# Kernel optimization log

Measured on AMD Instinct MI355X. Metric: run time of the kernel, lower is better.

## Reference

```python
import jax, jax.numpy as jnp
import numpy as np

B, INPUT_LEN, F_IN = 32, 4096, 256
N = B * INPUT_LEN          # 131072 total nodes in the flattened batch
E = 4_194_304              # ~avg degree 32
HID, OUT = 3, 1            # GCNConv(256->3) then GCNConv(3->1), per source code
PRED_LEN = 1024


def setup_inputs() -> dict:
    key = jax.random.key(0)
    k = jax.random.split(key, 5)
    node_features = jax.random.normal(k[0], (B, INPUT_LEN, F_IN), dtype=jnp.float32)
    # flattened, already-offset edge index (Batch.from_data_list result)
    edge_index = jax.random.randint(k[1], (2, E), 0, N, dtype=jnp.int32)
    W1 = jax.random.normal(k[2], (F_IN, HID), dtype=jnp.float32) / np.float32(np.sqrt(F_IN))
    b1 = jnp.zeros((HID,), dtype=jnp.float32)
    W2 = jax.random.normal(k[3], (HID, OUT), dtype=jnp.float32) / np.float32(np.sqrt(HID))
    b2 = jnp.zeros((OUT,), dtype=jnp.float32)
    return {"node_features": node_features, "W1": W1, "b1": b1, "W2": W2, "b2": b2,
            "edge_index": edge_index, "pred_len": PRED_LEN, "input_len": INPUT_LEN}


def _gcn_norm(edge_index, num_nodes, dtype):
    # PyG gcn_norm: add self-loops, deg over destination, symmetric deg^-1/2 norm
    loop = jnp.arange(num_nodes, dtype=edge_index.dtype)
    src = jnp.concatenate([edge_index[0], loop])
    dst = jnp.concatenate([edge_index[1], loop])
    deg = jax.ops.segment_sum(jnp.ones_like(src, dtype=dtype), dst, num_segments=num_nodes)
    dinv = jnp.where(deg > 0, jax.lax.rsqrt(deg), 0.0).astype(dtype)
    norm = dinv[src] * dinv[dst]  # [E+N]
    return src, dst, norm


def _gcn_conv(x, src, dst, norm, W, b, num_nodes):
    h = x @ W                              # [N, out] linear first (small out dim)
    msg = h[src] * norm[:, None]           # gather + scale per edge
    out = jax.ops.segment_sum(msg, dst, num_segments=num_nodes)  # scatter-add
    return out + b


def reference(node_features, W1, b1, W2, b2, edge_index, pred_len, input_len):
    n_nodes = node_features.shape[0] * node_features.shape[1]
    x = node_features.reshape(n_nodes, node_features.shape[2])
    src, dst, norm = _gcn_norm(edge_index, n_nodes, x.dtype)
    h = jax.nn.relu(_gcn_conv(x, src, dst, norm, W1, b1, n_nodes))
    h = _gcn_conv(h, src, dst, norm, W2, b2, n_nodes)
    h = h.reshape(-1, input_len, h.shape[1])   # [B, input_len, num_target]
    return h[:, :pred_len, :]
```

## Files before the change

### kernel.cpp

```cpp
#include <hip/hip_runtime.h>
#include <stdint.h>

#define F_IN 256
#define QSCALE 512.0f
#define QBIAS  8192
#define FMASK  0x1FFFFFull
#define H2Q    16384.0f
#define NBUK   256
#define BSH    9
#define BMASK  511u
#define LCAP   48
#define NCHUNK 512
#define EPB    8192
#define BSLOTS (NCHUNK * LCAP)
#define OVF_CAP 256
#define SENT   0xFFFFFFFFu
#define XBUF_SZ ((size_t)NBUK * BSLOTS * 4)
#define OVF_SZ  ((size_t)NBUK * OVF_CAP * 4)

__device__ __forceinline__ float bf2f(unsigned short u) {
    union { unsigned int i; float f; } v; v.i = ((unsigned int)u) << 16; return v.f;
}
__device__ __forceinline__ unsigned short f2bf(float f) {
    union { unsigned int i; float f; } v; v.f = f;
    unsigned int r = v.i + 0x7FFF + ((v.i >> 16) & 1);
    return (unsigned short)(r >> 16);
}
__device__ __forceinline__ unsigned long long packq(float v0, float v1, float v2) {
    int m0 = __float2int_rn(v0 * QSCALE);
    int m1 = __float2int_rn(v1 * QSCALE);
    int m2 = __float2int_rn(v2 * QSCALE);
    m0 = max(-4095, min(4095, m0));
    m1 = max(-4095, min(4095, m1));
    m2 = max(-4095, min(4095, m2));
    return (unsigned long long)(unsigned)(m0 + QBIAS)
         | ((unsigned long long)(unsigned)(m1 + QBIAS) << 21)
         | ((unsigned long long)(unsigned)(m2 + QBIAS) << 42);
}

__global__ void k_init(unsigned int* __restrict__ gcur,
                       const unsigned int* __restrict__ w1w, int* __restrict__ flag) {
    __shared__ int cnt;
    if (threadIdx.x == 0) cnt = 0;
    for (int i = threadIdx.x; i < NBUK * 16; i += blockDim.x) gcur[i] = 0u;
    __syncthreads();
    int local = 0;
    for (int i = threadIdx.x; i < 384; i += blockDim.x) {
        unsigned e = (w1w[i] >> 7) & 0xFF;
        if (e >= 100 && e <= 135) local++;
    }
    atomicAdd(&cnt, local);
    __syncthreads();
    if (threadIdx.x == 0) *flag = (2 * cnt < 384) ? 1 : 0;
}

__global__ void __launch_bounds__(256, 8)
k_gemv(const void* __restrict__ xv_, const void* __restrict__ w1_,
       unsigned short* __restrict__ h1out, const int* __restrict__ flag, int N) {
    __shared__ float wlds[F_IN * 3];
    int f32mode = *flag;
    if (f32mode) {
        const float* w = (const float*)w1_;
        for (int i = threadIdx.x; i < F_IN * 3; i += 256) wlds[i] = w[i];
    } else {
        const unsigned short* w = (const unsigned short*)w1_;
        for (int i = threadIdx.x; i < F_IN * 3; i += 256) wlds[i] = bf2f(w[i]);
    }
    __syncthreads();
    int wave = threadIdx.x >> 6, lane = threadIdx.x & 63;
    int g = lane >> 3, e = lane & 7;
    int row = blockIdx.x * 32 + wave * 8 + g;
    if (row >= N) return;
    float p0 = 0.f, p1 = 0.f, p2 = 0.f;
    if (f32mode) {
        const float4* xr = (const float4*)((const float*)xv_ + (size_t)row * F_IN);
        float4 xv[8];
        #pragma unroll
        for (int j = 0; j < 8; j++) xv[j] = xr[e + 8 * j];
        #pragma unroll
        for (int j = 0; j < 8; j++) {
            int f = 4 * e + 32 * j;
            const float4* wp = (const float4*)&wlds[f * 3];
            float4 wa = wp[0], wb = wp[1], wc = wp[2];
            p0 += xv[j].x*wa.x + xv[j].y*wa.w + xv[j].z*wb.z + xv[j].w*wc.y;
            p1 += xv[j].x*wa.y + xv[j].y*wb.x + xv[j].z*wb.w + xv[j].w*wc.z;
            p2 += xv[j].x*wa.z + xv[j].y*wb.y + xv[j].z*wc.x + xv[j].w*wc.w;
        }
    } else {
        const ushort4* xr = (const ushort4*)((const unsigned short*)xv_ + (size_t)row * F_IN);
        ushort4 xv[8];
        #pragma unroll
        for (int j = 0; j < 8; j++) xv[j] = xr[e + 8 * j];
        #pragma unroll
        for (int j = 0; j < 8; j++) {
            int f = 4 * e + 32 * j;
            const float4* wp = (const float4*)&wlds[f * 3];
            float4 wa = wp[0], wb = wp[1], wc = wp[2];
            float x0 = bf2f(xv[j].x), x1 = bf2f(xv[j].y),
                  x2 = bf2f(xv[j].z), x3 = bf2f(xv[j].w);
            p0 += x0*wa.x + x1*wa.w + x2*wb.z + x3*wc.y;
            p1 += x0*wa.y + x1*wb.x + x2*wb.w + x3*wc.z;
            p2 += x0*wa.z + x1*wb.y + x2*wc.x + x3*wc.w;
        }
    }
    #pragma unroll
    for (int m = 1; m < 8; m <<= 1) {
        p0 += __shfl_xor(p0, m, 64);
        p1 += __shfl_xor(p1, m, 64);
        p2 += __shfl_xor(p2, m, 64);
    }
    if (e == 0) {
        ushort4 o;
        o.x = f2bf(p0); o.y = f2bf(p1); o.z = f2bf(p2); o.w = 0;
        ((ushort4*)h1out)[row] = o;
    }
}

__global__ void __launch_bounds__(1024, 8)
k_bucket(const int* __restrict__ src, const int* __restrict__ dst,
         unsigned int* __restrict__ xbuf, unsigned int* __restrict__ ovf,
         unsigned int* __restrict__ gcur) {
    __shared__ unsigned int lbuf[NBUK][LCAP];
    __shared__ unsigned int lcnt[NBUK];
    int b = blockIdx.x;
    for (int i = threadIdx.x; i < NBUK; i += 1024) lcnt[i] = 0u;
    __syncthreads();
    int g4 = b * 2048 + threadIdx.x;
    int4 sa = ((const int4*)src)[g4];
    int4 da = ((const int4*)dst)[g4];
    int4 sb = ((const int4*)src)[g4 + 1024];
    int4 db = ((const int4*)dst)[g4 + 1024];
    int ss[8] = {sa.x, sa.y, sa.z, sa.w, sb.x, sb.y, sb.z, sb.w};
    int dd[8] = {da.x, da.y, da.z, da.w, db.x, db.y, db.z, db.w};
    #pragma unroll
    for (int u = 0; u < 8; u++) {
        unsigned p = ((unsigned)ss[u] << BSH) | ((unsigned)dd[u] & BMASK);
        int bk = ((unsigned)dd[u]) >> BSH;
        unsigned lp = atomicAdd(&lcnt[bk], 1u);
        if (lp < LCAP) lbuf[bk][lp] = p;
        else {
            unsigned g = atomicAdd(&gcur[bk << 4], 1u);
            if (g < OVF_CAP) ovf[(size_t)bk * OVF_CAP + g] = p;
        }
    }
    __syncthreads();
    int wave = threadIdx.x >> 6, lane = threadIdx.x & 63;
    #pragma unroll
    for (int k = 0; k < 16; k++) {
        int bk = wave * 16 + k;
        unsigned c = min(lcnt[bk], (unsigned)LCAP);
        if (lane < 12) {
            uint4 v = *(const uint4*)&lbuf[bk][lane * 4];
            unsigned s0 = lane * 4;
            uint4 o;
            o.x = (s0 + 0 < c) ? v.x : SENT;
            o.y = (s0 + 1 < c) ? v.y : SENT;
            o.z = (s0 + 2 < c) ? v.z : SENT;
            o.w = (s0 + 3 < c) ? v.w : SENT;
            ((uint4*)(xbuf + ((size_t)bk * NCHUNK + b) * LCAP))[lane] = o;
        }
    }
}

__global__ void __launch_bounds__(1024, 8)
k_hist_pack(const unsigned int* __restrict__ xbuf, const unsigned int* __restrict__ ovf,
            const unsigned int* __restrict__ gcur,
            unsigned char* __restrict__ deg8, float* __restrict__ dinv,
            unsigned long long* __restrict__ h1con) {
    __shared__ unsigned int cnt[512];
    int B = blockIdx.x;
    for (int i = threadIdx.x; i < 512; i += 1024) cnt[i] = 0u;
    __syncthreads();
    const uint4* bp = (const uint4*)(xbuf + (size_t)B * BSLOTS);
    for (int i = threadIdx.x; i < BSLOTS / 4; i += 1024) {
        uint4 v = bp[i];
        if (v.x != SENT) atomicAdd(&cnt[v.x & BMASK], 1u);
        if (v.y != SENT) atomicAdd(&cnt[v.y & BMASK], 1u);
        if (v.z != SENT) atomicAdd(&cnt[v.z & BMASK], 1u);
        if (v.w != SENT) atomicAdd(&cnt[v.w & BMASK], 1u);
    }
    unsigned oc = min(gcur[B << 4], (unsigned)OVF_CAP);
    for (unsigned i = threadIdx.x; i < oc; i += 1024)
        atomicAdd(&cnt[ovf[(size_t)B * OVF_CAP + i] & BMASK], 1u);
    __syncthreads();
    if (threadIdx.x < 512) {
        int n = (B << BSH) | threadIdx.x;
        unsigned deg = 1u + cnt[threadIdx.x];
        deg8[n] = (unsigned char)min(deg, 255u);
        float dv = rsqrtf((float)deg);
        dinv[n] = dv;
        ushort4 h = ((const ushort4*)h1con)[n];
        h1con[n] = packq(bf2f(h.x) * dv, bf2f(h.y) * dv, bf2f(h.z) * dv);
    }
}

__global__ void __launch_bounds__(1024, 8)
k_scat1_lin2(const unsigned int* __restrict__ xbuf, const unsigned int* __restrict__ ovf,
             const unsigned int* __restrict__ gcur,
             const unsigned long long* __restrict__ con,
             const unsigned char* __restrict__ deg8, const float* __restrict__ dinv,
             const void* __restrict__ b1_, const void* __restrict__ w2_,
             int* __restrict__ h2q, const int* __restrict__ flag) {
    __shared__ unsigned long long acc[512];
    int B = blockIdx.x;
    for (int i = threadIdx.x; i < 512; i += 1024) acc[i] = 0ull;
    __syncthreads();
    const uint4* bp = (const uint4*)(xbuf + (size_t)B * BSLOTS);
    for (int i = threadIdx.x; i < BSLOTS / 4; i += 1024) {
        uint4 v = bp[i];
        unsigned i0 = (v.x == SENT) ? 0u : (v.x >> BSH);
        unsigned i1 = (v.y == SENT) ? 0u : (v.y >> BSH);
        unsigned i2 = (v.z == SENT) ? 0u : (v.z >> BSH);
        unsigned i3 = (v.w == SENT) ? 0u : (v.w >> BSH);
        unsigned long long c0 = con[i0], c1 = con[i1], c2 = con[i2], c3 = con[i3];
        if (v.x != SENT) atomicAdd(&acc[v.x & BMASK], c0);
        if (v.y != SENT) atomicAdd(&acc[v.y & BMASK], c1);
        if (v.z != SENT) atomicAdd(&acc[v.z & BMASK], c2);
        if (v.w != SENT) atomicAdd(&acc[v.w & BMASK], c3);
    }
    unsigned oc = min(gcur[B << 4], (unsigned)OVF_CAP);
    for (unsigned i = threadIdx.x; i < oc; i += 1024) {
        unsigned p = ovf[(size_t)B * OVF_CAP + i];
        atomicAdd(&acc[p & BMASK], con[p >> BSH]);
    }
    __syncthreads();
    if (threadIdx.x < 512) {
        int n = (B << BSH) | threadIdx.x;
        int f32mode = *flag;
        float b10, b11, b12, w20, w21, w22;
        if (f32mode) {
            const float* b1 = (const float*)b1_; const float* w2 = (const float*)w2_;
            b10 = b1[0]; b11 = b1[1]; b12 = b1[2];
            w20 = w2[0]; w21 = w2[1]; w22 = w2[2];
        } else {
            const unsigned short* b1 = (const unsigned short*)b1_;
            const unsigned short* w2 = (const unsigned short*)w2_;
            b10 = bf2f(b1[0]); b11 = bf2f(b1[1]); b12 = bf2f(b1[2]);
            w20 = bf2f(w2[0]); w21 = bf2f(w2[1]); w22 = bf2f(w2[2]);
        }
        unsigned long long T = acc[threadIdx.x] + con[n];
        long long dbias = (long long)deg8[n] * QBIAS;
        float q = 1.0f / QSCALE;
        float s0 = (float)((long long)( T        & FMASK) - dbias) * q;
        float s1 = (float)((long long)((T >> 21) & FMASK) - dbias) * q;
        float s2 = (float)((long long)((T >> 42) & FMASK) - dbias) * q;
        float dv = dinv[n];
        float a0 = fmaxf(s0 * dv + b10, 0.0f);
        float a1 = fmaxf(s1 * dv + b11, 0.0f);
        float a2 = fmaxf(s2 * dv + b12, 0.0f);
        float h2 = (a0 * w20 + a1 * w21 + a2 * w22) * dv;
        h2q[n] = __float2int_rn(h2 * H2Q);
    }
}

__global__ void __launch_bounds__(1024, 8)
k_scat2_out(const unsigned int* __restrict__ xbuf, const unsigned int* __restrict__ ovf,
            const unsigned int* __restrict__ gcur,
            const int* __restrict__ h2q, const float* __restrict__ dinv,
            const void* __restrict__ b2_, void* __restrict__ out_,
            const int* __restrict__ flag) {
    __shared__ int acc[512];
    int ob = blockIdx.x;
    int B = ((ob >> 1) << 3) | (ob & 1);
    for (int i = threadIdx.x; i < 512; i += 1024) acc[i] = 0;
    __syncthreads();
    const uint4* bp = (const uint4*)(xbuf + (size_t)B * BSLOTS);
    for (int i = threadIdx.x; i < BSLOTS / 4; i += 1024) {
        uint4 v = bp[i];
        unsigned i0 = (v.x == SENT) ? 0u : (v.x >> BSH);
        unsigned i1 = (v.y == SENT) ? 0u : (v.y >> BSH);
        unsigned i2 = (v.z == SENT) ? 0u : (v.z >> BSH);
        unsigned i3 = (v.w == SENT) ? 0u : (v.w >> BSH);
        int h0 = h2q[i0], h1 = h2q[i1], h2v = h2q[i2], h3 = h2q[i3];
        if (v.x != SENT) atomicAdd(&acc[v.x & BMASK], h0);
        if (v.y != SENT) atomicAdd(&acc[v.y & BMASK], h1);
        if (v.z != SENT) atomicAdd(&acc[v.z & BMASK], h2v);
        if (v.w != SENT) atomicAdd(&acc[v.w & BMASK], h3);
    }
    unsigned oc = min(gcur[B << 4], (unsigned)OVF_CAP);
    for (unsigned i = threadIdx.x; i < oc; i += 1024) {
        unsigned p = ovf[(size_t)B * OVF_CAP + i];
        atomicAdd(&acc[p & BMASK], h2q[p >> BSH]);
    }
    __syncthreads();
    if (threadIdx.x < 512) {
        int i = threadIdx.x;
        int n = (B << BSH) | i;
        int f32mode = *flag;
        float b2 = f32mode ? ((const float*)b2_)[0] : bf2f(((const unsigned short*)b2_)[0]);
        int S = h2q[n] + acc[i];
        float v = (float)S * (1.0f / H2Q) * dinv[n] + b2;
        int t = ((B >> 3) << 10) | ((B & 1) << 9) | i;
        if (f32mode) ((float*)out_)[t] = v;
        else         ((unsigned short*)out_)[t] = f2bf(v);
    }
}

extern "C" void kernel_launch(void* const* d_in, const int* in_sizes, int n_in,
                              void* d_out, int out_size, void* d_ws, size_t ws_size,
                              hipStream_t stream) {
    void*       x   = d_in[0];
    const void* w1  = d_in[1];
    const void* b1  = d_in[2];
    const void* w2  = d_in[3];
    const void* b2  = d_in[4];
    const int* eidx = (const int*)d_in[5];

    const int N = in_sizes[0] / F_IN;
    const int E = in_sizes[5] / 2;
    const int* src = eidx;
    const int* dst = eidx + E;

    char* ws = (char*)d_ws;
    unsigned char*      deg8  = (unsigned char*)(ws);
    float*              dinv  = (float*)(ws + (size_t)N);
    unsigned long long* h1con = (unsigned long long*)(ws + (size_t)5*N);
    int*                h2q   = (int*)(ws + (size_t)13*N);
    int*                flag  = (int*)(ws + (size_t)17*N);
    unsigned int*       gcur  = (unsigned int*)(ws + (size_t)17*N + 64);

    bool big_ws = ws_size >= ((size_t)(4u << 20) + XBUF_SZ + OVF_SZ);
    char* scratch = big_ws ? (ws + (4u << 20)) : (char*)x;
    unsigned int* xbuf = (unsigned int*)scratch;
    unsigned int* ovf  = (unsigned int*)(scratch + XBUF_SZ);

    int gemvB = N / 32;
    k_init<<<1, 256, 0, stream>>>(gcur, (const unsigned int*)w1, flag);
    if (big_ws) {
        k_bucket<<<NCHUNK, 1024, 0, stream>>>(src, dst, xbuf, ovf, gcur);
        k_gemv<<<gemvB, 256, 0, stream>>>(x, w1, (unsigned short*)h1con, flag, N);
    } else {
        k_gemv<<<gemvB, 256, 0, stream>>>(x, w1, (unsigned short*)h1con, flag, N);
        k_bucket<<<NCHUNK, 1024, 0, stream>>>(src, dst, xbuf, ovf, gcur);
    }
    k_hist_pack  <<<NBUK, 1024, 0, stream>>>(xbuf, ovf, gcur, deg8, dinv, h1con);
    k_scat1_lin2 <<<NBUK, 1024, 0, stream>>>(xbuf, ovf, gcur, h1con, deg8, dinv,
                                             b1, w2, h2q, flag);
    k_scat2_out  <<<64, 1024, 0, stream>>>(xbuf, ovf, gcur, h2q, dinv, b2,
                                           d_out, flag);
}
```

Before: 285.7 us.

## Use persistent wave-per-row GEMV, spread bucket flush across lanes, relax launch bounds

The first-layer GEMV switches from eight rows per wave with LDS weight reads to a grid-stride loop where each wave handles one row at a time. Each lane keeps its slice of W1 in registers, and the row is reduced with a full 64-lane shuffle. The bucket kernel's flush of local buffers to global memory now spreads the 16 buckets times 12 uint4 slots across all lanes, where before only 12 of 64 lanes were active. Launch bounds on the 1024-thread kernels drop the minimum blocks per CU from 8 to 2, which may give the compiler more registers. The risks are that each row now needs a longer shuffle chain and has less memory-level parallelism per wave.

```diff
diff --git a/kernel.cpp b/kernel.cpp
--- a/kernel.cpp
+++ b/kernel.cpp
@@ -67,56 +67,39 @@
         for (int i = threadIdx.x; i < F_IN * 3; i += 256) wlds[i] = bf2f(w[i]);
     }
     __syncthreads();
-    int wave = threadIdx.x >> 6, lane = threadIdx.x & 63;
-    int g = lane >> 3, e = lane & 7;
-    int row = blockIdx.x * 32 + wave * 8 + g;
-    if (row >= N) return;
-    float p0 = 0.f, p1 = 0.f, p2 = 0.f;
-    if (f32mode) {
-        const float4* xr = (const float4*)((const float*)xv_ + (size_t)row * F_IN);
-        float4 xv[8];
+    int lane = threadIdx.x & 63;
+    float4 wa = ((const float4*)wlds)[3 * lane + 0];
+    float4 wb = ((const float4*)wlds)[3 * lane + 1];
+    float4 wc = ((const float4*)wlds)[3 * lane + 2];
+    int gw = blockIdx.x * 4 + (threadIdx.x >> 6);
+    int nw = gridDim.x * 4;
+    for (int row = gw; row < N; row += nw) {
+        float x0, x1, x2, x3;
+        if (f32mode) {
+            float4 v = ((const float4*)((const float*)xv_ + (size_t)row * F_IN))[lane];
+            x0 = v.x; x1 = v.y; x2 = v.z; x3 = v.w;
+        } else {
+            ushort4 v = ((const ushort4*)((const unsigned short*)xv_ + (size_t)row * F_IN))[lane];
+            x0 = bf2f(v.x); x1 = bf2f(v.y); x2 = bf2f(v.z); x3 = bf2f(v.w);
+        }
+        float p0 = x0*wa.x + x1*wa.w + x2*wb.z + x3*wc.y;
+        float p1 = x0*wa.y + x1*wb.x + x2*wb.w + x3*wc.z;
+        float p2 = x0*wa.z + x1*wb.y + x2*wc.x + x3*wc.w;
         #pragma unroll
-        for (int j = 0; j < 8; j++) xv[j] = xr[e + 8 * j];
-        #pragma unroll
-        for (int j = 0; j < 8; j++) {
-            int f = 4 * e + 32 * j;
-            const float4* wp = (const float4*)&wlds[f * 3];
-            float4 wa = wp[0], wb = wp[1], wc = wp[2];
-            p0 += xv[j].x*wa.x + xv[j].y*wa.w + xv[j].z*wb.z + xv[j].w*wc.y;
-            p1 += xv[j].x*wa.y + xv[j].y*wb.x + xv[j].z*wb.w + xv[j].w*wc.z;
-            p2 += xv[j].x*wa.z + xv[j].y*wb.y + xv[j].z*wc.x + xv[j].w*wc.w;
-        }
-    } else {
-        const ushort4* xr = (const ushort4*)((const unsigned short*)xv_ + (size_t)row * F_IN);
-        ushort4 xv[8];
-        #pragma unroll
-        for (int j = 0; j < 8; j++) xv[j] = xr[e + 8 * j];
-        #pragma unroll
-        for (int j = 0; j < 8; j++) {
-            int f = 4 * e + 32 * j;
-            const float4* wp = (const float4*)&wlds[f * 3];
-            float4 wa = wp[0], wb = wp[1], wc = wp[2];
-            float x0 = bf2f(xv[j].x), x1 = bf2f(xv[j].y),
-                  x2 = bf2f(xv[j].z), x3 = bf2f(xv[j].w);
-            p0 += x0*wa.x + x1*wa.w + x2*wb.z + x3*wc.y;
-            p1 += x0*wa.y + x1*wb.x + x2*wb.w + x3*wc.z;
-            p2 += x0*wa.z + x1*wb.y + x2*wc.x + x3*wc.w;
-        }
-    }
-    #pragma unroll
-    for (int m = 1; m < 8; m <<= 1) {
-        p0 += __shfl_xor(p0, m, 64);
-        p1 += __shfl_xor(p1, m, 64);
-        p2 += __shfl_xor(p2, m, 64);
-    }
-    if (e == 0) {
-        ushort4 o;
-        o.x = f2bf(p0); o.y = f2bf(p1); o.z = f2bf(p2); o.w = 0;
-        ((ushort4*)h1out)[row] = o;
-    }
-}
-
-__global__ void __launch_bounds__(1024, 8)
+        for (int m = 1; m < 64; m <<= 1) {
+            p0 += __shfl_xor(p0, m, 64);
+            p1 += __shfl_xor(p1, m, 64);
+            p2 += __shfl_xor(p2, m, 64);
+        }
+        if (lane == 0) {
+            ushort4 o;
+            o.x = f2bf(p0); o.y = f2bf(p1); o.z = f2bf(p2); o.w = 0;
+            ((ushort4*)h1out)[row] = o;
+        }
+    }
+}
+
+__global__ void __launch_bounds__(1024, 2)
 k_bucket(const int* __restrict__ src, const int* __restrict__ dst,
          unsigned int* __restrict__ xbuf, unsigned int* __restrict__ ovf,
          unsigned int* __restrict__ gcur) {
@@ -145,24 +128,25 @@
     }
     __syncthreads();
     int wave = threadIdx.x >> 6, lane = threadIdx.x & 63;
+    int bk0 = wave * 16;
     #pragma unroll
-    for (int k = 0; k < 16; k++) {
-        int bk = wave * 16 + k;
+    for (int k = 0; k < 3; k++) {
+        int idx = k * 64 + lane;
+        int bo = idx / 12, sl = idx - bo * 12;
+        int bk = bk0 + bo;
         unsigned c = min(lcnt[bk], (unsigned)LCAP);
-        if (lane < 12) {
-            uint4 v = *(const uint4*)&lbuf[bk][lane * 4];
-            unsigned s0 = lane * 4;
-            uint4 o;
-            o.x = (s0 + 0 < c) ? v.x : SENT;
-            o.y = (s0 + 1 < c) ? v.y : SENT;
-            o.z = (s0 + 2 < c) ? v.z : SENT;
-            o.w = (s0 + 3 < c) ? v.w : SENT;
-            ((uint4*)(xbuf + ((size_t)bk * NCHUNK + b) * LCAP))[lane] = o;
-        }
-    }
-}
-
-__global__ void __launch_bounds__(1024, 8)
+        uint4 v = *(const uint4*)&lbuf[bk][sl * 4];
+        unsigned s0 = sl * 4;
+        uint4 o;
+        o.x = (s0 + 0 < c) ? v.x : SENT;
+        o.y = (s0 + 1 < c) ? v.y : SENT;
+        o.z = (s0 + 2 < c) ? v.z : SENT;
+        o.w = (s0 + 3 < c) ? v.w : SENT;
+        ((uint4*)(xbuf + ((size_t)bk * NCHUNK + b) * LCAP))[sl] = o;
+    }
+}
+
+__global__ void __launch_bounds__(1024, 2)
 k_hist_pack(const unsigned int* __restrict__ xbuf, const unsigned int* __restrict__ ovf,
             const unsigned int* __restrict__ gcur,
             unsigned char* __restrict__ deg8, float* __restrict__ dinv,
@@ -194,7 +178,7 @@
     }
 }
 
-__global__ void __launch_bounds__(1024, 8)
+__global__ void __launch_bounds__(1024, 2)
 k_scat1_lin2(const unsigned int* __restrict__ xbuf, const unsigned int* __restrict__ ovf,
              const unsigned int* __restrict__ gcur,
              const unsigned long long* __restrict__ con,
@@ -253,7 +237,7 @@
     }
 }
 
-__global__ void __launch_bounds__(1024, 8)
+__global__ void __launch_bounds__(1024, 2)
 k_scat2_out(const unsigned int* __restrict__ xbuf, const unsigned int* __restrict__ ovf,
             const unsigned int* __restrict__ gcur,
             const int* __restrict__ h2q, const float* __restrict__ dinv,
@@ -324,13 +308,12 @@
     unsigned int* xbuf = (unsigned int*)scratch;
     unsigned int* ovf  = (unsigned int*)(scratch + XBUF_SZ);
 
-    int gemvB = N / 32;
     k_init<<<1, 256, 0, stream>>>(gcur, (const unsigned int*)w1, flag);
     if (big_ws) {
         k_bucket<<<NCHUNK, 1024, 0, stream>>>(src, dst, xbuf, ovf, gcur);
-        k_gemv<<<gemvB, 256, 0, stream>>>(x, w1, (unsigned short*)h1con, flag, N);
+        k_gemv<<<2048, 256, 0, stream>>>(x, w1, (unsigned short*)h1con, flag, N);
     } else {
-        k_gemv<<<gemvB, 256, 0, stream>>>(x, w1, (unsigned short*)h1con, flag, N);
+        k_gemv<<<2048, 256, 0, stream>>>(x, w1, (unsigned short*)h1con, flag, N);
         k_bucket<<<NCHUNK, 1024, 0, stream>>>(src, dst, xbuf, ovf, gcur);
     }
     k_hist_pack  <<<NBUK, 1024, 0, stream>>>(xbuf, ovf, gcur, deg8, dinv, h1con);
```

Result: faster. 277.6 us (-2.8%).
